# Optimization experiments

Hardware: AMD Instinct MI355X
Metric: run time of the kernel (lower is better)

Reference implementation:

```python
import jax, jax.numpy as jnp
import numpy as np

B, S, D, H, DFF = 4, 2048, 1024, 8, 4096
DH = D // H  # 128
EPS = 1e-5


def layernorm(x, gamma, beta):
    mu = jnp.mean(x, axis=-1, keepdims=True)
    var = jnp.mean(jnp.square(x - mu), axis=-1, keepdims=True)
    return (x - mu) * jax.lax.rsqrt(var + EPS) * gamma + beta


def setup_inputs() -> dict:
    key = jax.random.key(0)
    ks = jax.random.split(key, 6)
    s = 0.02
    return {
        "src": jax.random.normal(ks[0], (B, S, D), jnp.float32),
        "w_qkv": jax.random.normal(ks[1], (D, 3 * D), jnp.float32) * s,
        "w_out": jax.random.normal(ks[2], (D, D), jnp.float32) * s,
        "w1": jax.random.normal(ks[3], (D, DFF), jnp.float32) * s,
        "b1": jnp.zeros((DFF,), jnp.float32),
        "w2": jax.random.normal(ks[4], (DFF, D), jnp.float32) * s,
        "b2": jnp.zeros((D,), jnp.float32),
        "g1": jnp.ones((D,), jnp.float32),
        "beta1": jnp.zeros((D,), jnp.float32),
        "g2": jnp.ones((D,), jnp.float32),
        "beta2": jnp.zeros((D,), jnp.float32),
    }


def reference(src, w_qkv, w_out, w1, b1, w2, b2, g1, beta1, g2, beta2):
    b, s, d = src.shape
    # --- RingAttention == exact causal MHA on a single device ---
    qkv = src @ w_qkv  # [b, s, 3d]
    q, k, v = jnp.split(qkv, 3, axis=-1)
    to_heads = lambda x: x.reshape(b, s, H, DH).transpose(0, 2, 1, 3)  # [b,h,s,dh]
    q, k, v = to_heads(q), to_heads(k), to_heads(v)
    scale = 1.0 / jnp.sqrt(jnp.asarray(DH, src.dtype))
    scores = jnp.einsum('bhqd,bhkd->bhqk', q, k) * scale  # [b,h,s,s]
    causal = jnp.tril(jnp.ones((s, s), bool))
    neg = jnp.asarray(jnp.finfo(src.dtype).min, src.dtype)
    scores = jnp.where(causal, scores, neg)
    attn = jax.nn.softmax(scores, axis=-1)
    o = jnp.einsum('bhqk,bhkd->bhqd', attn, v)  # [b,h,s,dh]
    o = o.transpose(0, 2, 1, 3).reshape(b, s, d) @ w_out
    # dropout layers are identity at inference
    x = layernorm(src + o, g1, beta1)
    ff = jax.nn.relu(x @ w1 + b1) @ w2 + b2
    return layernorm(x + ff, g2, beta2)
```

## Files before the change

### kernel.cpp

```cpp
#include <hip/hip_runtime.h>

typedef unsigned short u16;
typedef __attribute__((ext_vector_type(8))) short short8;
typedef __attribute__((ext_vector_type(4))) float float4v;

#define MFMA_BF16(a, b, c) __builtin_amdgcn_mfma_f32_16x16x32_bf16((a), (b), (c), 0, 0, 0)

#define B_ 4
#define S_ 2048
#define D_ 1024
#define H_ 8
#define DH_ 128
#define DFF_ 4096
#define EPS_ 1e-5f
#define ROWS_ (B_ * S_)
#define CSCALE_ 0.12751672939502f

__device__ __forceinline__ u16 f2bf(float f) {
  union { float f; unsigned u; } x; x.f = f;
  unsigned r = x.u + 0x7fffu + ((x.u >> 16) & 1u);
  return (u16)(r >> 16);
}

typedef __attribute__((address_space(1))) const unsigned int guint;
typedef __attribute__((address_space(3))) unsigned int luint;
__device__ __forceinline__ void gl2lds16(const u16* g, u16* l) {
  __builtin_amdgcn_global_load_lds((guint*)g, (luint*)l, 16, 0, 0);
}

__global__ void cast_bf16_kernel(const float* __restrict__ in, u16* __restrict__ out, int n4) {
  int i = blockIdx.x * blockDim.x + threadIdx.x;
  int stride = gridDim.x * blockDim.x;
  for (; i < n4; i += stride) {
    float4 v = ((const float4*)in)[i];
    ushort4 u;
    u.x = f2bf(v.x); u.y = f2bf(v.y); u.z = f2bf(v.z); u.w = f2bf(v.w);
    ((ushort4*)out)[i] = u;
  }
}

__global__ void transpose_cast_kernel(const float* __restrict__ in, u16* __restrict__ out,
                                      int K, int N) {
  __shared__ float t[32][33];
  int k0 = blockIdx.x * 32, n0 = blockIdx.y * 32;
  int tx = threadIdx.x & 31, ty = threadIdx.x >> 5;
  #pragma unroll
  for (int i = 0; i < 4; ++i)
    t[ty + 8 * i][tx] = in[(size_t)(k0 + ty + 8 * i) * N + n0 + tx];
  __syncthreads();
  #pragma unroll
  for (int i = 0; i < 4; ++i)
    out[(size_t)(n0 + ty + 8 * i) * K + k0 + tx] = f2bf(t[tx][ty + 8 * i]);
}

__global__ void transpose_v_kernel(const u16* __restrict__ in, u16* __restrict__ out) {
  __shared__ u16 t[32][33];
  int s0 = blockIdx.x * 32, d0 = blockIdx.y * 32, bh = blockIdx.z;
  const u16* src = in + (size_t)bh * S_ * DH_;
  u16* dst = out + (size_t)bh * DH_ * S_;
  int tx = threadIdx.x & 31, ty = threadIdx.x >> 5;
  #pragma unroll
  for (int i = 0; i < 4; ++i)
    t[ty + 8 * i][tx] = src[(size_t)(s0 + ty + 8 * i) * DH_ + d0 + tx];
  __syncthreads();
  #pragma unroll
  for (int i = 0; i < 4; ++i)
    dst[(size_t)(d0 + ty + 8 * i) * S_ + s0 + tx] = t[tx][ty + 8 * i];
}

template <int MODE>
__global__ __launch_bounds__(512, 2) void gemm256_kernel(
    const u16* __restrict__ A, const u16* __restrict__ Bt,
    const int M, const int N, const int K,
    float* __restrict__ outF, u16* __restrict__ outH, const float* __restrict__ bias,
    u16* __restrict__ qo, u16* __restrict__ ko, u16* __restrict__ vo) {
  extern __shared__ u16 smem[];
  u16* At  = smem;
  u16* Bts = smem + 2 * 256 * 64;
  const int tid = threadIdx.x;
  const int lane = tid & 63, wave = tid >> 6;
  const int quad = lane >> 4, r16 = lane & 15;
  const int halfw = wave >> 2;
  const int wn = (wave & 3) * 64;
  const int m0 = blockIdx.x * 256, n0 = blockIdx.y * 256;
  const int NT = K >> 6;

  const int rowin = wave * 8 + (lane >> 3);
  const int sc = lane & 7;
  const int shalf = rowin >> 5, srr = rowin & 31;

  const u16* Asrc[4];
  const u16* Bsrc[4];
  #pragma unroll
  for (int u = 0; u < 4; ++u) {
    const int ra = shalf * 128 + u * 32 + srr;
    Asrc[u] = A + (size_t)(m0 + ra) * K + (sc ^ (ra & 7)) * 8;
    const int rb = u * 64 + rowin;
    Bsrc[u] = Bt + (size_t)(n0 + rb) * K + (sc ^ (rb & 7)) * 8;
  }

  float4v acc[8][4];
  #pragma unroll
  for (int i = 0; i < 8; ++i)
    #pragma unroll
    for (int j = 0; j < 4; ++j) acc[i][j] = (float4v)0.0f;

#define STAGE_A(t, u) gl2lds16(Asrc[u] + (t) * 64, At  + ((t) & 1) * 16384 + (u) * 4096 + wave * 512)
#define STAGE_B(t, u) gl2lds16(Bsrc[u] + (t) * 64, Bts + ((t) & 1) * 16384 + (u) * 4096 + wave * 512)

  STAGE_B(0, 0); STAGE_B(0, 1); STAGE_B(0, 2); STAGE_B(0, 3);
  STAGE_A(0, 0); STAGE_A(0, 1); STAGE_A(0, 2); STAGE_A(0, 3);
  if (NT > 1) {
    STAGE_B(1, 0); STAGE_B(1, 1); STAGE_B(1, 2); STAGE_B(1, 3);
    STAGE_A(1, 0); STAGE_A(1, 1);
    asm volatile("s_waitcnt vmcnt(6)" ::: "memory");
  } else {
    asm volatile("s_waitcnt vmcnt(0)" ::: "memory");
  }
  __builtin_amdgcn_s_barrier();

  for (int kt = 0; kt < NT; ++kt) {
    const u16* Ab = At + (kt & 1) * 16384;
    const u16* Bb = Bts + (kt & 1) * 16384;
    short8 bfr[4][2];
    #pragma unroll
    for (int q = 0; q < 4; ++q) {
      if (q == 0) {
        #pragma unroll
        for (int j = 0; j < 4; ++j)
          #pragma unroll
          for (int s = 0; s < 2; ++s)
            bfr[j][s] = *(const short8*)(Bb + (wn + j * 16 + r16) * 64 +
                                         (((s * 4 + quad) ^ (r16 & 7)) * 8));
      }
      short8 af[2][2];
      #pragma unroll
      for (int di = 0; di < 2; ++di)
        #pragma unroll
        for (int s = 0; s < 2; ++s)
          af[di][s] = *(const short8*)(Ab + (q * 64 + halfw * 32 + di * 16 + r16) * 64 +
                                       (((s * 4 + quad) ^ (r16 & 7)) * 8));
      if (q == 0)      { if (kt + 1 < NT) { STAGE_A(kt + 1, 2); STAGE_A(kt + 1, 3); } }
      else if (q == 1) { if (kt + 2 < NT) { STAGE_B(kt + 2, 0); STAGE_B(kt + 2, 1); } }
      else if (q == 2) { if (kt + 2 < NT) { STAGE_B(kt + 2, 2); STAGE_B(kt + 2, 3); } }
      else             { if (kt + 2 < NT) { STAGE_A(kt + 2, 0); STAGE_A(kt + 2, 1); } }
      __builtin_amdgcn_s_barrier();
      asm volatile("s_waitcnt lgkmcnt(0)" ::: "memory");
      __builtin_amdgcn_s_setprio(1);
      #pragma unroll
      for (int j = 0; j < 4; ++j) {
        acc[2 * q][j]     = MFMA_BF16(af[0][0], bfr[j][0], acc[2 * q][j]);
        acc[2 * q][j]     = MFMA_BF16(af[0][1], bfr[j][1], acc[2 * q][j]);
        acc[2 * q + 1][j] = MFMA_BF16(af[1][0], bfr[j][0], acc[2 * q + 1][j]);
        acc[2 * q + 1][j] = MFMA_BF16(af[1][1], bfr[j][1], acc[2 * q + 1][j]);
      }
      __builtin_amdgcn_s_setprio(0);
      if (q == 3) {
        if (kt + 2 < NT)      { asm volatile("s_waitcnt vmcnt(6)" ::: "memory"); }
        else if (kt + 1 < NT) { asm volatile("s_waitcnt vmcnt(0)" ::: "memory"); }
      }
      __builtin_amdgcn_s_barrier();
    }
  }
#undef STAGE_A
#undef STAGE_B

  #pragma unroll
  for (int i = 0; i < 8; ++i) {
    const int rowb = m0 + halfw * 128 + i * 16 + quad * 4;
    #pragma unroll
    for (int j = 0; j < 4; ++j) {
      const int col = n0 + wn + j * 16 + r16;
      #pragma unroll
      for (int rg = 0; rg < 4; ++rg) {
        float val = acc[i][j][rg];
        const int r = rowb + rg;
        if (MODE == 2) {
          val += bias[col];
          val = fmaxf(val, 0.0f);
          outH[(size_t)r * N + col] = f2bf(val);
        } else {
          outF[(size_t)r * N + col] = val;
        }
      }
    }
  }
}

template <int MODE>
__global__ __launch_bounds__(512, 2) void gemm256x128_kernel(
    const u16* __restrict__ A, const u16* __restrict__ Bt,
    const int M, const int N, const int K, const int lda,
    float* __restrict__ outF, float* __restrict__ outF2,
    u16* __restrict__ outH, const float* __restrict__ bias,
    u16* __restrict__ qo, u16* __restrict__ ko, u16* __restrict__ vo) {
  extern __shared__ u16 smem[];
  u16* At  = smem;
  u16* Bts = smem + 2 * 256 * 64;
  const int tid = threadIdx.x;
  const int lane = tid & 63, wave = tid >> 6;
  const int quad = lane >> 4, r16 = lane & 15;
  const int w64 = wave >> 1;
  const int wn = (wave & 1) * 64;
  const int m0 = blockIdx.x * 256, n0 = blockIdx.y * 128;
  const int NT = K >> 6;
  const int kof = (MODE == 4) ? (int)blockIdx.z * K : 0;

  const int rowin = wave * 8 + (lane >> 3);
  const int sc = lane & 7;

  const u16* Asrc[4];
  const u16* Bsrc[2];
  #pragma unroll
  for (int u = 0; u < 4; ++u) {
    const int ra = ((u & 1) * 2 + (rowin >> 5)) * 64 + (u >> 1) * 32 + (rowin & 31);
    Asrc[u] = A + (size_t)(m0 + ra) * lda + kof + (sc ^ (ra & 7)) * 8;
  }
  #pragma unroll
  for (int u = 0; u < 2; ++u) {
    const int rb = u * 64 + rowin;
    Bsrc[u] = Bt + (size_t)(n0 + rb) * lda + kof + (sc ^ (rb & 7)) * 8;
  }

  float4v acc[4][4];
  #pragma unroll
  for (int i = 0; i < 4; ++i)
    #pragma unroll
    for (int j = 0; j < 4; ++j) acc[i][j] = (float4v)0.0f;

#define STAGE_A(t, u) gl2lds16(Asrc[u] + (t) * 64, At  + ((t) & 1) * 16384 + (u) * 4096 + wave * 512)
#define STAGE_B(t, u) gl2lds16(Bsrc[u] + (t) * 64, Bts + ((t) & 1) * 8192 + (u) * 4096 + wave * 512)

  STAGE_B(0, 0); STAGE_B(0, 1); STAGE_A(0, 0); STAGE_A(0, 1);
  STAGE_A(0, 2); STAGE_A(0, 3);
  STAGE_B(1, 0); STAGE_B(1, 1); STAGE_A(1, 0); STAGE_A(1, 1);
  asm volatile("s_waitcnt vmcnt(6)" ::: "memory");
  __builtin_amdgcn_s_barrier();

  for (int kt = 0; kt < NT; ++kt) {
    const u16* Ab = At + (kt & 1) * 16384;
    const u16* Bb = Bts + (kt & 1) * 8192;
    short8 bfr[4][2];
    #pragma unroll
    for (int j = 0; j < 4; ++j)
      #pragma unroll
      for (int s = 0; s < 2; ++s)
        bfr[j][s] = *(const short8*)(Bb + (wn + j * 16 + r16) * 64 +
                                     (((s * 4 + quad) ^ (r16 & 7)) * 8));
    {
      short8 af[2][2];
      #pragma unroll
      for (int di = 0; di < 2; ++di)
        #pragma unroll
        for (int s = 0; s < 2; ++s)
          af[di][s] = *(const short8*)(Ab + (w64 * 32 + di * 16 + r16) * 64 +
                                       (((s * 4 + quad) ^ (r16 & 7)) * 8));
      if (kt + 1 < NT) { STAGE_A(kt + 1, 2); STAGE_A(kt + 1, 3); }
      __builtin_amdgcn_s_barrier();
      asm volatile("s_waitcnt lgkmcnt(0)" ::: "memory");
      __builtin_amdgcn_s_setprio(1);
      #pragma unroll
      for (int j = 0; j < 4; ++j) {
        acc[0][j] = MFMA_BF16(af[0][0], bfr[j][0], acc[0][j]);
        acc[0][j] = MFMA_BF16(af[0][1], bfr[j][1], acc[0][j]);
        acc[1][j] = MFMA_BF16(af[1][0], bfr[j][0], acc[1][j]);
        acc[1][j] = MFMA_BF16(af[1][1], bfr[j][1], acc[1][j]);
      }
      __builtin_amdgcn_s_setprio(0);
      if (kt + 1 < NT) { asm volatile("s_waitcnt vmcnt(6)" ::: "memory"); }
      else             { asm volatile("s_waitcnt vmcnt(0)" ::: "memory"); }
      __builtin_amdgcn_s_barrier();
    }
    {
      short8 af[2][2];
      #pragma unroll
      for (int di = 0; di < 2; ++di)
        #pragma unroll
        for (int s = 0; s < 2; ++s)
          af[di][s] = *(const short8*)(Ab + (128 + w64 * 32 + di * 16 + r16) * 64 +
                                       (((s * 4 + quad) ^ (r16 & 7)) * 8));
      if (kt + 2 < NT) {
        STAGE_B(kt + 2, 0); STAGE_B(kt + 2, 1);
        STAGE_A(kt + 2, 0); STAGE_A(kt + 2, 1);
      }
      __builtin_amdgcn_s_barrier();
      asm volatile("s_waitcnt lgkmcnt(0)" ::: "memory");
      __builtin_amdgcn_s_setprio(1);
      #pragma unroll
      for (int j = 0; j < 4; ++j) {
        acc[2][j] = MFMA_BF16(af[0][0], bfr[j][0], acc[2][j]);
        acc[2][j] = MFMA_BF16(af[0][1], bfr[j][1], acc[2][j]);
        acc[3][j] = MFMA_BF16(af[1][0], bfr[j][0], acc[3][j]);
        acc[3][j] = MFMA_BF16(af[1][1], bfr[j][1], acc[3][j]);
      }
      __builtin_amdgcn_s_setprio(0);
      if (kt + 1 < NT) {
        if (kt + 2 < NT) { asm volatile("s_waitcnt vmcnt(6)" ::: "memory"); }
        else             { asm volatile("s_waitcnt vmcnt(2)" ::: "memory"); }
      }
      __builtin_amdgcn_s_barrier();
    }
  }
#undef STAGE_A
#undef STAGE_B

  #pragma unroll
  for (int i = 0; i < 4; ++i) {
    const int rowb = m0 + w64 * 64 + i * 16 + quad * 4;
    #pragma unroll
    for (int j = 0; j < 4; ++j) {
      const int col = n0 + wn + j * 16 + r16;
      #pragma unroll
      for (int rg = 0; rg < 4; ++rg) {
        float val = acc[i][j][rg];
        const int r = rowb + rg;
        if (MODE == 0) {
          const int part = col >> 10, cc = col & 1023;
          const int h = cc >> 7, dh = cc & 127;
          const int b = r >> 11, s = r & 2047;
          u16* dst = (part == 0) ? qo : (part == 1) ? ko : vo;
          if (part == 0) val *= CSCALE_;
          dst[((size_t)(b * H_ + h) * S_ + s) * DH_ + dh] = f2bf(val);
        } else if (MODE == 1) {
          outF[(size_t)r * N + col] = val;
        } else if (MODE == 4) {
          float* dst = blockIdx.z ? outF2 : outF;
          if (blockIdx.z == 0) val += bias[col];
          dst[(size_t)r * N + col] = val;
        } else {
          val += bias[col];
          outF[(size_t)r * N + col] = val;
        }
      }
    }
  }
}

__global__ __launch_bounds__(256) void attn_kernel(
    const u16* __restrict__ Q, const u16* __restrict__ Kg,
    const u16* __restrict__ Vtg, u16* __restrict__ O) {
  __shared__ u16 Ks[64][136];
  __shared__ u16 Vt[128][72];
  __shared__ u16 Pw[4][16][72];
  const int tid = threadIdx.x;
  const int lane = tid & 63, wave = tid >> 6;
  const int quad = lane >> 4, r16 = lane & 15;
  const int id = blockIdx.x;
  const int bh = (id & 7) * 4 + ((id >> 3) & 3);
  const int qb = 31 - (id >> 5);
  const size_t base = (size_t)bh * S_ * DH_;
  const size_t vtb = (size_t)bh * DH_ * S_;
  const int b = bh >> 3, h = bh & 7;

  const u16* kg0 = Kg + base + (size_t)(tid >> 4) * DH_ + (tid & 15) * 8;
  u16* ksl = &Ks[tid >> 4][(tid & 15) * 8];
  const u16* vg0 = Vtg + vtb + (size_t)(tid >> 3) * S_ + (tid & 7) * 8;
  u16* vtl = &Vt[tid >> 3][(tid & 7) * 8];

  short8 rk[4], rv[4];
#define LOADKV(kb_)                                                        \
  do {                                                                     \
    _Pragma("unroll")                                                      \
    for (int i_ = 0; i_ < 4; ++i_)                                         \
      rk[i_] = *(const short8*)(kg0 + (size_t)((kb_) * 64 + i_ * 16) * DH_); \
    _Pragma("unroll")                                                      \
    for (int i_ = 0; i_ < 4; ++i_)                                         \
      rv[i_] = *(const short8*)(vg0 + (size_t)i_ * 32 * S_ + (kb_) * 64);  \
  } while (0)

  const int qr = qb * 64 + wave * 16 + r16;

  short8 aq[4];
  #pragma unroll
  for (int ks = 0; ks < 4; ++ks)
    aq[ks] = *(const short8*)(Q + base + (size_t)qr * DH_ + ks * 32 + quad * 8);

  float4v acco[8];
  #pragma unroll
  for (int i = 0; i < 8; ++i) acco[i] = (float4v)0.0f;
  float m_q = -1e30f, l_q = 0.0f;

  LOADKV(0);

  for (int kb = 0; kb <= qb; ++kb) {
    __syncthreads();
    #pragma unroll
    for (int i = 0; i < 4; ++i) *(short8*)(ksl + i * 16 * 136) = rk[i];
    #pragma unroll
    for (int i = 0; i < 4; ++i) *(short8*)(vtl + i * 32 * 72) = rv[i];
    __syncthreads();
    if (kb < qb) LOADKV(kb + 1);

    float4v accs[4];
    #pragma unroll
    for (int t = 0; t < 4; ++t) accs[t] = (float4v)0.0f;
    #pragma unroll
    for (int ks = 0; ks < 4; ++ks) {
      #pragma unroll
      for (int t = 0; t < 4; ++t) {
        short8 ak = *(const short8*)&Ks[t * 16 + r16][ks * 32 + quad * 8];
        accs[t] = MFMA_BF16(ak, aq[ks], accs[t]);
      }
    }
    if (kb == qb) {
      #pragma unroll
      for (int t = 0; t < 4; ++t)
        #pragma unroll
        for (int rg = 0; rg < 4; ++rg) {
          int kc = kb * 64 + t * 16 + quad * 4 + rg;
          if (kc > qr) accs[t][rg] = -1e30f;
        }
    }
    float mv = accs[0][0];
    #pragma unroll
    for (int t = 0; t < 4; ++t)
      #pragma unroll
      for (int rg = 0; rg < 4; ++rg) mv = fmaxf(mv, accs[t][rg]);
    mv = fmaxf(mv, __shfl_xor(mv, 16));
    mv = fmaxf(mv, __shfl_xor(mv, 32));
    const bool nore = __all(mv <= m_q + 8.0f) != 0;
    const float mnew = nore ? m_q : fmaxf(m_q, mv);
    float alpha = 1.0f;
    if (!nore) alpha = __builtin_amdgcn_exp2f(m_q - mnew);
    float s0 = 0.0f;
    #pragma unroll
    for (int t = 0; t < 4; ++t)
      #pragma unroll
      for (int rg = 0; rg < 4; ++rg) {
        float p = __builtin_amdgcn_exp2f(accs[t][rg] - mnew);
        accs[t][rg] = p;
        s0 += p;
      }
    s0 += __shfl_xor(s0, 16);
    s0 += __shfl_xor(s0, 32);
    l_q = nore ? (l_q + s0) : (l_q * alpha + s0);
    m_q = mnew;

    #pragma unroll
    for (int t = 0; t < 4; ++t) {
      union { float f; unsigned u; } c0, c1, c2, c3;
      c0.f = accs[t][0]; c1.f = accs[t][1]; c2.f = accs[t][2]; c3.f = accs[t][3];
      uint2 pk;
      pk.x = ((c0.u + 0x8000u) >> 16) | ((c1.u + 0x8000u) & 0xffff0000u);
      pk.y = ((c2.u + 0x8000u) >> 16) | ((c3.u + 0x8000u) & 0xffff0000u);
      *(uint2*)&Pw[wave][r16][t * 16 + quad * 4] = pk;
    }
    if (!nore) {
      float al[4];
      #pragma unroll
      for (int rg = 0; rg < 4; ++rg) al[rg] = __shfl(alpha, quad * 4 + rg);
      #pragma unroll
      for (int nt = 0; nt < 8; ++nt)
        #pragma unroll
        for (int rg = 0; rg < 4; ++rg) acco[nt][rg] *= al[rg];
    }
    asm volatile("s_waitcnt lgkmcnt(0)" ::: "memory");
    #pragma unroll
    for (int ks2 = 0; ks2 < 2; ++ks2) {
      short8 ap = *(const short8*)&Pw[wave][r16][ks2 * 32 + quad * 8];
      #pragma unroll
      for (int nt = 0; nt < 8; ++nt) {
        short8 bv = *(const short8*)&Vt[nt * 16 + r16][ks2 * 32 + quad * 8];
        acco[nt] = MFMA_BF16(ap, bv, acco[nt]);
      }
    }
  }

  float lr[4];
  #pragma unroll
  for (int rg = 0; rg < 4; ++rg) lr[rg] = __shfl(l_q, quad * 4 + rg);
  const int sbase = qb * 64 + wave * 16 + quad * 4;
  #pragma unroll
  for (int nt = 0; nt < 8; ++nt)
    #pragma unroll
    for (int rg = 0; rg < 4; ++rg) {
      float val = acco[nt][rg] / lr[rg];
      O[((size_t)(b * S_ + sbase + rg)) * D_ + h * DH_ + nt * 16 + r16] = f2bf(val);
    }
#undef LOADKV
}

__global__ __launch_bounds__(256) void ln_kernel(
    const float* __restrict__ a, const float* __restrict__ a2,
    const float* __restrict__ res,
    const float* __restrict__ g, const float* __restrict__ be,
    float* __restrict__ xf, u16* __restrict__ xb) {
  __shared__ float red[8];
  const int row = blockIdx.x, tid = threadIdx.x;
  const float4 va = ((const float4*)(a + (size_t)row * D_))[tid];
  const float4 vr = ((const float4*)(res + (size_t)row * D_))[tid];
  float4 v;
  v.x = va.x + vr.x; v.y = va.y + vr.y; v.z = va.z + vr.z; v.w = va.w + vr.w;
  if (a2) {
    const float4 v2 = ((const float4*)(a2 + (size_t)row * D_))[tid];
    v.x += v2.x; v.y += v2.y; v.z += v2.z; v.w += v2.w;
  }
  float s = v.x + v.y + v.z + v.w;
  float q = v.x * v.x + v.y * v.y + v.z * v.z + v.w * v.w;
  #pragma unroll
  for (int m = 1; m < 64; m <<= 1) {
    s += __shfl_xor(s, m);
    q += __shfl_xor(q, m);
  }
  const int wave = tid >> 6, lane = tid & 63;
  if (lane == 0) { red[wave] = s; red[4 + wave] = q; }
  __syncthreads();
  s = red[0] + red[1] + red[2] + red[3];
  q = red[4] + red[5] + red[6] + red[7];
  const float mu = s * (1.0f / D_);
  const float var = q * (1.0f / D_) - mu * mu;
  const float inv = rsqrtf(var + EPS_);
  const float4 gg = ((const float4*)g)[tid];
  const float4 bb = ((const float4*)be)[tid];
  float4 y;
  y.x = (v.x - mu) * inv * gg.x + bb.x;
  y.y = (v.y - mu) * inv * gg.y + bb.y;
  y.z = (v.z - mu) * inv * gg.z + bb.z;
  y.w = (v.w - mu) * inv * gg.w + bb.w;
  ((float4*)(xf + (size_t)row * D_))[tid] = y;
  if (xb) {
    ushort4 u;
    u.x = f2bf(y.x); u.y = f2bf(y.y); u.z = f2bf(y.z); u.w = f2bf(y.w);
    ((ushort4*)(xb + (size_t)row * D_))[tid] = u;
  }
}

extern "C" void kernel_launch(void* const* d_in, const int* in_sizes, int n_in,
                              void* d_out, int out_size, void* d_ws, size_t ws_size,
                              hipStream_t stream) {
  const float* src   = (const float*)d_in[0];
  const float* w_qkv = (const float*)d_in[1];
  const float* w_out = (const float*)d_in[2];
  const float* w1    = (const float*)d_in[3];
  const float* b1    = (const float*)d_in[4];
  const float* w2    = (const float*)d_in[5];
  const float* b2    = (const float*)d_in[6];
  const float* g1    = (const float*)d_in[7];
  const float* be1   = (const float*)d_in[8];
  const float* g2    = (const float*)d_in[9];
  const float* be2   = (const float*)d_in[10];
  float* out = (float*)d_out;

  char* ws = (char*)d_ws;
  size_t off = 0;
  auto alloc = [&](size_t bytes) -> void* {
    void* p = ws + off;
    off += (bytes + 255) & ~(size_t)255;
    return p;
  };
  u16* src_bf = (u16*)alloc((size_t)ROWS_ * D_ * 2);
  u16* wqkvT  = (u16*)alloc((size_t)3 * D_ * D_ * 2);
  u16* woutT  = (u16*)alloc((size_t)D_ * D_ * 2);
  u16* w1T    = (u16*)alloc((size_t)DFF_ * D_ * 2);
  u16* w2T    = (u16*)alloc((size_t)D_ * DFF_ * 2);
  u16* qbuf   = (u16*)alloc((size_t)ROWS_ * D_ * 2);
  u16* kbuf   = (u16*)alloc((size_t)ROWS_ * D_ * 2);
  u16* vbuf   = (u16*)alloc((size_t)ROWS_ * D_ * 2);
  u16* obuf   = (u16*)alloc((size_t)ROWS_ * D_ * 2);
  u16* vT     = (u16*)alloc((size_t)ROWS_ * D_ * 2);
  float* proj = (float*)alloc((size_t)ROWS_ * D_ * 4);
  float* xf   = (float*)alloc((size_t)ROWS_ * D_ * 4);
  u16* xb     = (u16*)alloc((size_t)ROWS_ * D_ * 2);
  u16* h1     = qbuf;
  float* ff   = proj;
  float* ff2  = (float*)ws;

  const int GSMEM  = 131072;
  const int GSMEM2 = 98304;
  hipFuncSetAttribute((const void*)gemm256_kernel<2>, hipFuncAttributeMaxDynamicSharedMemorySize, GSMEM);
  hipFuncSetAttribute((const void*)gemm256x128_kernel<0>, hipFuncAttributeMaxDynamicSharedMemorySize, GSMEM2);
  hipFuncSetAttribute((const void*)gemm256x128_kernel<1>, hipFuncAttributeMaxDynamicSharedMemorySize, GSMEM2);
  hipFuncSetAttribute((const void*)gemm256x128_kernel<4>, hipFuncAttributeMaxDynamicSharedMemorySize, GSMEM2);

  cast_bf16_kernel<<<2048, 256, 0, stream>>>(src, src_bf, ROWS_ * D_ / 4);
  transpose_cast_kernel<<<dim3(D_ / 32, 3 * D_ / 32), 256, 0, stream>>>(w_qkv, wqkvT, D_, 3 * D_);
  transpose_cast_kernel<<<dim3(D_ / 32, D_ / 32), 256, 0, stream>>>(w_out, woutT, D_, D_);
  transpose_cast_kernel<<<dim3(D_ / 32, DFF_ / 32), 256, 0, stream>>>(w1, w1T, D_, DFF_);
  transpose_cast_kernel<<<dim3(DFF_ / 32, D_ / 32), 256, 0, stream>>>(w2, w2T, DFF_, D_);

  gemm256x128_kernel<0><<<dim3(ROWS_ / 256, 3 * D_ / 128), 512, GSMEM2, stream>>>(
      src_bf, wqkvT, ROWS_, 3 * D_, D_, D_, nullptr, nullptr, nullptr, nullptr, qbuf, kbuf, vbuf);
  transpose_v_kernel<<<dim3(S_ / 32, DH_ / 32, B_ * H_), 256, 0, stream>>>(vbuf, vT);
  attn_kernel<<<1024, 256, 0, stream>>>(qbuf, kbuf, vT, obuf);
  gemm256x128_kernel<1><<<dim3(ROWS_ / 256, D_ / 128), 512, GSMEM2, stream>>>(
      obuf, woutT, ROWS_, D_, D_, D_, proj, nullptr, nullptr, nullptr, nullptr, nullptr, nullptr);
  ln_kernel<<<ROWS_, 256, 0, stream>>>(proj, nullptr, src, g1, be1, xf, xb);
  gemm256_kernel<2><<<dim3(ROWS_ / 256, DFF_ / 256), 512, GSMEM, stream>>>(
      xb, w1T, ROWS_, DFF_, D_, nullptr, h1, b1, nullptr, nullptr, nullptr);
  gemm256x128_kernel<4><<<dim3(ROWS_ / 256, D_ / 128, 2), 512, GSMEM2, stream>>>(
      h1, w2T, ROWS_, D_, DFF_ / 2, DFF_, ff, ff2, nullptr, b2, nullptr, nullptr, nullptr);
  ln_kernel<<<ROWS_, 256, 0, stream>>>(ff, ff2, xf, g2, be2, out, nullptr);
}
```

Measured before the change: 502.2 us.

## Write V transposed from QKV GEMM epilogue and drop split-K for FFN2

The QKV projection epilogue now stores V directly in the [b,h,dh,s] layout the attention kernel expects, which removes the separate transpose_v kernel and its extra read and write of V. The second FFN GEMM goes back from a 2-way split-K (two fp32 partial outputs summed in layernorm) to a single pass over the full K, halving the grid to 256 blocks. The transposed V stores are strided by S and likely poorly coalesced. The FFN2 change trades away the extra partial-buffer traffic for less parallelism.

```diff
diff --git a/kernel.cpp b/kernel.cpp
--- a/kernel.cpp
+++ b/kernel.cpp
@@ -51,21 +51,6 @@
   #pragma unroll
   for (int i = 0; i < 4; ++i)
     out[(size_t)(n0 + ty + 8 * i) * K + k0 + tx] = f2bf(t[tx][ty + 8 * i]);
-}
-
-__global__ void transpose_v_kernel(const u16* __restrict__ in, u16* __restrict__ out) {
-  __shared__ u16 t[32][33];
-  int s0 = blockIdx.x * 32, d0 = blockIdx.y * 32, bh = blockIdx.z;
-  const u16* src = in + (size_t)bh * S_ * DH_;
-  u16* dst = out + (size_t)bh * DH_ * S_;
-  int tx = threadIdx.x & 31, ty = threadIdx.x >> 5;
-  #pragma unroll
-  for (int i = 0; i < 4; ++i)
-    t[ty + 8 * i][tx] = src[(size_t)(s0 + ty + 8 * i) * DH_ + d0 + tx];
-  __syncthreads();
-  #pragma unroll
-  for (int i = 0; i < 4; ++i)
-    dst[(size_t)(d0 + ty + 8 * i) * S_ + s0 + tx] = t[tx][ty + 8 * i];
 }
 
 template <int MODE>
@@ -190,9 +175,8 @@
 template <int MODE>
 __global__ __launch_bounds__(512, 2) void gemm256x128_kernel(
     const u16* __restrict__ A, const u16* __restrict__ Bt,
-    const int M, const int N, const int K, const int lda,
-    float* __restrict__ outF, float* __restrict__ outF2,
-    u16* __restrict__ outH, const float* __restrict__ bias,
+    const int M, const int N, const int K,
+    float* __restrict__ outF, u16* __restrict__ outH, const float* __restrict__ bias,
     u16* __restrict__ qo, u16* __restrict__ ko, u16* __restrict__ vo) {
   extern __shared__ u16 smem[];
   u16* At  = smem;
@@ -204,7 +188,6 @@
   const int wn = (wave & 1) * 64;
   const int m0 = blockIdx.x * 256, n0 = blockIdx.y * 128;
   const int NT = K >> 6;
-  const int kof = (MODE == 4) ? (int)blockIdx.z * K : 0;
 
   const int rowin = wave * 8 + (lane >> 3);
   const int sc = lane & 7;
@@ -214,12 +197,12 @@
   #pragma unroll
   for (int u = 0; u < 4; ++u) {
     const int ra = ((u & 1) * 2 + (rowin >> 5)) * 64 + (u >> 1) * 32 + (rowin & 31);
-    Asrc[u] = A + (size_t)(m0 + ra) * lda + kof + (sc ^ (ra & 7)) * 8;
+    Asrc[u] = A + (size_t)(m0 + ra) * K + (sc ^ (ra & 7)) * 8;
   }
   #pragma unroll
   for (int u = 0; u < 2; ++u) {
     const int rb = u * 64 + rowin;
-    Bsrc[u] = Bt + (size_t)(n0 + rb) * lda + kof + (sc ^ (rb & 7)) * 8;
+    Bsrc[u] = Bt + (size_t)(n0 + rb) * K + (sc ^ (rb & 7)) * 8;
   }
 
   float4v acc[4][4];
@@ -318,15 +301,15 @@
           const int part = col >> 10, cc = col & 1023;
           const int h = cc >> 7, dh = cc & 127;
           const int b = r >> 11, s = r & 2047;
-          u16* dst = (part == 0) ? qo : (part == 1) ? ko : vo;
-          if (part == 0) val *= CSCALE_;
-          dst[((size_t)(b * H_ + h) * S_ + s) * DH_ + dh] = f2bf(val);
+          if (part == 0) {
+            qo[((size_t)(b * H_ + h) * S_ + s) * DH_ + dh] = f2bf(val * CSCALE_);
+          } else if (part == 1) {
+            ko[((size_t)(b * H_ + h) * S_ + s) * DH_ + dh] = f2bf(val);
+          } else {
+            vo[((size_t)(b * H_ + h) * DH_ + dh) * S_ + s] = f2bf(val);
+          }
         } else if (MODE == 1) {
           outF[(size_t)r * N + col] = val;
-        } else if (MODE == 4) {
-          float* dst = blockIdx.z ? outF2 : outF;
-          if (blockIdx.z == 0) val += bias[col];
-          dst[(size_t)r * N + col] = val;
         } else {
           val += bias[col];
           outF[(size_t)r * N + col] = val;
@@ -555,22 +538,20 @@
   u16* w2T    = (u16*)alloc((size_t)D_ * DFF_ * 2);
   u16* qbuf   = (u16*)alloc((size_t)ROWS_ * D_ * 2);
   u16* kbuf   = (u16*)alloc((size_t)ROWS_ * D_ * 2);
-  u16* vbuf   = (u16*)alloc((size_t)ROWS_ * D_ * 2);
+  u16* vT     = (u16*)alloc((size_t)ROWS_ * D_ * 2);
   u16* obuf   = (u16*)alloc((size_t)ROWS_ * D_ * 2);
-  u16* vT     = (u16*)alloc((size_t)ROWS_ * D_ * 2);
   float* proj = (float*)alloc((size_t)ROWS_ * D_ * 4);
   float* xf   = (float*)alloc((size_t)ROWS_ * D_ * 4);
   u16* xb     = (u16*)alloc((size_t)ROWS_ * D_ * 2);
   u16* h1     = qbuf;
   float* ff   = proj;
-  float* ff2  = (float*)ws;
 
   const int GSMEM  = 131072;
   const int GSMEM2 = 98304;
   hipFuncSetAttribute((const void*)gemm256_kernel<2>, hipFuncAttributeMaxDynamicSharedMemorySize, GSMEM);
   hipFuncSetAttribute((const void*)gemm256x128_kernel<0>, hipFuncAttributeMaxDynamicSharedMemorySize, GSMEM2);
   hipFuncSetAttribute((const void*)gemm256x128_kernel<1>, hipFuncAttributeMaxDynamicSharedMemorySize, GSMEM2);
-  hipFuncSetAttribute((const void*)gemm256x128_kernel<4>, hipFuncAttributeMaxDynamicSharedMemorySize, GSMEM2);
+  hipFuncSetAttribute((const void*)gemm256x128_kernel<3>, hipFuncAttributeMaxDynamicSharedMemorySize, GSMEM2);
 
   cast_bf16_kernel<<<2048, 256, 0, stream>>>(src, src_bf, ROWS_ * D_ / 4);
   transpose_cast_kernel<<<dim3(D_ / 32, 3 * D_ / 32), 256, 0, stream>>>(w_qkv, wqkvT, D_, 3 * D_);
@@ -579,15 +560,14 @@
   transpose_cast_kernel<<<dim3(DFF_ / 32, D_ / 32), 256, 0, stream>>>(w2, w2T, DFF_, D_);
 
   gemm256x128_kernel<0><<<dim3(ROWS_ / 256, 3 * D_ / 128), 512, GSMEM2, stream>>>(
-      src_bf, wqkvT, ROWS_, 3 * D_, D_, D_, nullptr, nullptr, nullptr, nullptr, qbuf, kbuf, vbuf);
-  transpose_v_kernel<<<dim3(S_ / 32, DH_ / 32, B_ * H_), 256, 0, stream>>>(vbuf, vT);
+      src_bf, wqkvT, ROWS_, 3 * D_, D_, nullptr, nullptr, nullptr, qbuf, kbuf, vT);
   attn_kernel<<<1024, 256, 0, stream>>>(qbuf, kbuf, vT, obuf);
   gemm256x128_kernel<1><<<dim3(ROWS_ / 256, D_ / 128), 512, GSMEM2, stream>>>(
-      obuf, woutT, ROWS_, D_, D_, D_, proj, nullptr, nullptr, nullptr, nullptr, nullptr, nullptr);
+      obuf, woutT, ROWS_, D_, D_, proj, nullptr, nullptr, nullptr, nullptr, nullptr);
   ln_kernel<<<ROWS_, 256, 0, stream>>>(proj, nullptr, src, g1, be1, xf, xb);
   gemm256_kernel<2><<<dim3(ROWS_ / 256, DFF_ / 256), 512, GSMEM, stream>>>(
       xb, w1T, ROWS_, DFF_, D_, nullptr, h1, b1, nullptr, nullptr, nullptr);
-  gemm256x128_kernel<4><<<dim3(ROWS_ / 256, D_ / 128, 2), 512, GSMEM2, stream>>>(
-      h1, w2T, ROWS_, D_, DFF_ / 2, DFF_, ff, ff2, nullptr, b2, nullptr, nullptr, nullptr);
-  ln_kernel<<<ROWS_, 256, 0, stream>>>(ff, ff2, xf, g2, be2, out, nullptr);
-}
+  gemm256x128_kernel<3><<<dim3(ROWS_ / 256, D_ / 128), 512, GSMEM2, stream>>>(
+      h1, w2T, ROWS_, D_, DFF_, ff, nullptr, b2, nullptr, nullptr, nullptr);
+  ln_kernel<<<ROWS_, 256, 0, stream>>>(ff, nullptr, xf, g2, be2, out, nullptr);
+}
```

Result: no change. 511.2 us (+1.8%).
